# Kernel tuning notes

Measured on AMD Instinct MI355X. Metric: run time of the kernel, lower is better.

Reference implementation:

```python
import jax, jax.numpy as jnp
import numpy as np

B, T, D = 64, 128, 512  # batch, seq_len, d_model == memory_dim


def setup_inputs() -> dict:
    key = jax.random.key(0)
    ks = jax.random.split(key, 14)
    bound = 1.0 / np.sqrt(D)  # nn.Linear / kaiming_uniform(a=sqrt(5)) bound for fan_in=D
    u = lambda k, shape: jax.random.uniform(k, shape, jnp.float32, -bound, bound)
    return {
        "x": jax.random.normal(ks[0], (B, T, D), jnp.float32),
        "W_Q": u(ks[1], (D, D)),
        "W_K": u(ks[2], (D, D)),
        "W_V": u(ks[3], (D, D)),
        "theta_w": u(ks[4], (1, D)), "theta_b": u(ks[5], (1,)),
        "eta_w": u(ks[6], (1, D)), "eta_b": u(ks[7], (1,)),
        "alpha_w": u(ks[8], (1, D)), "alpha_b": u(ks[9], (1,)),
        "W1": u(ks[10], (D, D)), "b1": u(ks[11], (D,)),
        "W2": u(ks[12], (D, D)), "b2": u(ks[13], (D,)),
    }


def _run(x, W_Q, W_K, W_V, theta_w, theta_b, eta_w, eta_b, alpha_w, alpha_b,
         W1, b1, W2, b2):
    LO, HI = 1e-10, 1e10  # loss clamp range (grad passes through strictly inside)
    Bn, Tn, Dn = x.shape
    N = Bn * Dn  # mse_loss 'mean' normalizer over (batch, memory_dim)

    def step(carry, x_t):  # x_t: (B, D)
        cW1, cb1, cW2, cb2, M1w, M1b, M2w, M2b = carry
        # read path: q -> 2-layer memory MLP (relu, then linear)
        q = x_t @ W_Q.T
        mem = jax.nn.relu(q @ cW1.T + cb1) @ cW2.T + cb2
        # per-step scalar gates: mean over batch of sigmoid(proj(x_t))
        theta = jnp.mean(jax.nn.sigmoid(x_t @ theta_w.T + theta_b))
        eta = jnp.mean(jax.nn.sigmoid(x_t @ eta_w.T + eta_b))
        alpha = jnp.mean(jax.nn.sigmoid(x_t @ alpha_w.T + alpha_b))
        # write path: grad of clamped mean MSE( MLP(k), v ) wrt memory weights
        k = x_t @ W_K.T
        v = x_t @ W_V.T
        h_pre = k @ cW1.T + cb1
        h = jax.nn.relu(h_pre)
        out = h @ cW2.T + cb2
        diff = out - v
        loss = jnp.mean(diff * diff)
        pt = jnp.where((loss >= LO) & (loss <= HI), 1.0, 0.0)  # clamp passthrough
        dout = (pt * 2.0 / N) * diff                            # (B, D)
        gW2 = dout.T @ h
        gb2 = dout.sum(0)
        dpre = jnp.where(h_pre > 0, dout @ cW2, 0.0)
        gW1 = dpre.T @ k
        gb1 = dpre.sum(0)
        # momentum + weight decay update
        M1w = eta * M1w - theta * gW1
        M1b = eta * M1b - theta * gb1
        M2w = eta * M2w - theta * gW2
        M2b = eta * M2b - theta * gb2
        nW1 = (1.0 - alpha) * cW1 + M1w
        nb1 = (1.0 - alpha) * cb1 + M1b
        nW2 = (1.0 - alpha) * cW2 + M2w
        nb2 = (1.0 - alpha) * cb2 + M2b
        return (nW1, nb1, nW2, nb2, M1w, M1b, M2w, M2b), mem

    carry0 = (W1, b1, W2, b2,
              jnp.zeros_like(W1), jnp.zeros_like(b1),
              jnp.zeros_like(W2), jnp.zeros_like(b2))
    _, mem_seq = jax.lax.scan(step, carry0, jnp.swapaxes(x, 0, 1))  # (T, B, D)
    return jnp.swapaxes(mem_seq, 0, 1)  # (B, T, D)


def reference(x, W_Q, W_K, W_V, theta_w, theta_b, eta_w, eta_b, alpha_w, alpha_b,
              W1, b1, W2, b2):
    outputs = _run(x, W_Q, W_K, W_V, theta_w, theta_b, eta_w, eta_b,
                   alpha_w, alpha_b, W1, b1, W2, b2)
    # original returns (outputs, memory_outputs), which are identical tensors
    return (outputs, outputs)
```

## Files before the change

kernel.cpp:

```cpp
#include <hip/hip_runtime.h>
#include <stdint.h>


typedef __attribute__((ext_vector_type(8))) short short8;
typedef __attribute__((ext_vector_type(4))) float floatx4;

#define GBLK 16
#define SC_AGENT __HIP_MEMORY_SCOPE_AGENT

__device__ inline floatx4 mfma_bf16(short8 a, short8 b, floatx4 c) {
  return __builtin_amdgcn_mfma_f32_16x16x32_bf16(a, b, c, 0, 0, 0);
}
__device__ inline unsigned short f2bf(float f) {
  unsigned u = __float_as_uint(f);
  u += 0x7fffu + ((u >> 16) & 1u);
  return (unsigned short)(u >> 16);
}
__device__ inline float bf2f(unsigned short h) {
  return __uint_as_float(((unsigned)h) << 16);
}
__device__ inline short8 ldbf8(const unsigned short* p) {
  return *reinterpret_cast<const short8*>(p);
}
__device__ inline void stg16_sc(unsigned short* p, short8 v) {
  asm volatile("global_store_dwordx4 %0, %1, off sc0 sc1"
               :: "v"(p), "v"(v) : "memory");
}
__device__ inline void vmwait() {
  asm volatile("s_waitcnt vmcnt(0)" ::: "memory");
}
__device__ inline short8 ld16_sc(const unsigned short* p) {
  union { unsigned long long u[2]; short8 s; } c;
  c.u[0] = __hip_atomic_load(reinterpret_cast<const unsigned long long*>(p),
                             __ATOMIC_RELAXED, SC_AGENT);
  c.u[1] = __hip_atomic_load(reinterpret_cast<const unsigned long long*>(p + 4),
                             __ATOMIC_RELAXED, SC_AGENT);
  return c.s;
}
__device__ inline short8 pack8(const float* p) {
  float4 a = *reinterpret_cast<const float4*>(p);
  float4 b = *reinterpret_cast<const float4*>(p + 4);
  short8 r;
  r[0] = (short)f2bf(a.x); r[1] = (short)f2bf(a.y);
  r[2] = (short)f2bf(a.z); r[3] = (short)f2bf(a.w);
  r[4] = (short)f2bf(b.x); r[5] = (short)f2bf(b.y);
  r[6] = (short)f2bf(b.z); r[7] = (short)f2bf(b.w);
  return r;
}

__device__ inline void gridbar(unsigned* ctr, unsigned& ep) {
  vmwait();
  __syncthreads();
  if (threadIdx.x == 0) {
    __hip_atomic_fetch_add(ctr, 1u, __ATOMIC_RELAXED, SC_AGENT);
    const unsigned target = (ep + 1u) * GBLK;
    while (__hip_atomic_load(ctr, __ATOMIC_RELAXED, SC_AGENT) < target)
      __builtin_amdgcn_s_sleep(1);
  }
  ++ep;
  __syncthreads();
}

__global__ __launch_bounds__(256) void qkv_kernel(
    const float* __restrict__ x, const float* __restrict__ WQ,
    const float* __restrict__ WK, const float* __restrict__ WV,
    unsigned short* __restrict__ qb, unsigned short* __restrict__ kb,
    unsigned short* __restrict__ vb, unsigned short* __restrict__ kbT) {
  const int tid = threadIdx.x;
  const int lane = tid & 63, w = tid >> 6;
  const int quad = lane >> 4, l16 = lane & 15;
  const int Mbase = blockIdx.x * 128;
  const int Nbase = blockIdx.y * 128;
  const int z = blockIdx.z;
  const float* W = (z == 0) ? WQ : (z == 1) ? WK : WV;
  unsigned short* dst = (z == 0) ? qb : (z == 1) ? kb : vb;

  floatx4 acc[2][8];
  for (int a = 0; a < 2; ++a)
    for (int n = 0; n < 8; ++n) acc[a][n] = (floatx4){0.f, 0.f, 0.f, 0.f};

  const int r0 = Mbase + w * 32 + l16;
  for (int ks = 0; ks < 16; ++ks) {
    const int k0 = ks * 32 + quad * 8;
    short8 a0 = pack8(x + (size_t)r0 * 512 + k0);
    short8 a1 = pack8(x + (size_t)(r0 + 16) * 512 + k0);
    for (int n = 0; n < 8; ++n) {
      short8 b = pack8(W + (size_t)(Nbase + n * 16 + l16) * 512 + k0);
      acc[0][n] = mfma_bf16(a0, b, acc[0][n]);
      acc[1][n] = mfma_bf16(a1, b, acc[1][n]);
    }
  }
  for (int tm = 0; tm < 2; ++tm)
    for (int n = 0; n < 8; ++n)
      for (int rr = 0; rr < 4; ++rr) {
        int row = Mbase + w * 32 + tm * 16 + quad * 4 + rr;
        int col = Nbase + n * 16 + l16;
        int b = row >> 7, t = row & 127;
        unsigned short val = f2bf(acc[tm][n][rr]);
        dst[((size_t)(t * 64 + b) << 9) + col] = val;
        if (z == 1) kbT[((size_t)(t * 512 + col) << 6) + b] = val;
      }
}

__global__ __launch_bounds__(256) void gates_kernel(
    const float* __restrict__ x,
    const float* __restrict__ tw, const float* __restrict__ tb,
    const float* __restrict__ ew, const float* __restrict__ eb,
    const float* __restrict__ aw, const float* __restrict__ ab,
    float* __restrict__ gates, float* __restrict__ lossAcc,
    unsigned* __restrict__ ctr) {
  const int t = blockIdx.x, tid = threadIdx.x;
  __shared__ float red[192];
  if (tid < 192) {
    int g = tid >> 6, b = tid & 63;
    const float* wr = (g == 0) ? tw : (g == 1) ? ew : aw;
    float bias = (g == 0) ? tb[0] : (g == 1) ? eb[0] : ab[0];
    const float* xr = x + ((size_t)b * 128 + t) * 512;
    float s = 0.f;
    for (int i = 0; i < 512; i += 4) {
      float4 xv = *reinterpret_cast<const float4*>(xr + i);
      float4 wv = *reinterpret_cast<const float4*>(wr + i);
      s += xv.x * wv.x + xv.y * wv.y + xv.z * wv.z + xv.w * wv.w;
    }
    red[tid] = 1.f / (1.f + expf(-(s + bias)));
  }
  if (tid == 192) lossAcc[t] = 0.f;
  if (tid == 193 && t == 0) *ctr = 0u;
  __syncthreads();
  if (tid < 3) {
    float s = 0.f;
    for (int i = 0; i < 64; ++i) s += red[tid * 64 + i];
    gates[tid * 128 + t] = s * (1.f / 64.f);
  }
}

__global__ __launch_bounds__(512, 2) void scan_kernel(
    const unsigned short* __restrict__ qb, const unsigned short* __restrict__ kb,
    const unsigned short* __restrict__ vb, const unsigned short* __restrict__ kbT,
    const float* __restrict__ gates, float* lossAcc, unsigned* ctr,
    const float* __restrict__ inW1, const float* __restrict__ inb1,
    const float* __restrict__ inW2, const float* __restrict__ inb2,
    unsigned short* W2T, unsigned short* RcG, unsigned short* hT,
    unsigned short* dout_rm, float* __restrict__ out) {
  __shared__ unsigned short sW1[32 * 520];
  __shared__ unsigned short sW2[32 * 520];
  __shared__ unsigned short sWT[512 * 40];
  __shared__ unsigned short shl[32 * 72];
  __shared__ unsigned short sdt[32 * 72];
  __shared__ unsigned short sdp[32 * 72];
  __shared__ unsigned short sStA[128 * 32];
  __shared__ unsigned short sDR[64 * 32];
  __shared__ float sOutF[64 * 32];
  __shared__ float b1loc[32], b2loc[32], mb1[32], mb2[32];

  const int tid = threadIdx.x, bid = blockIdx.x;
  const int lane = tid & 63, w = tid >> 6;
  const int quad = lane >> 4, l16 = lane & 15;
  const int J = bid * 32;
  const int mt = w & 1, ng = w >> 1;
  const int mtc = w & 3, ntc = w >> 2;
  unsigned ep = 0;

  float w1s[32], m1s[32], w2s[32], m2s[32];
#pragma unroll
  for (int g = 0; g < 8; ++g) {
    unsigned short tp[4];
#pragma unroll
    for (int rr = 0; rr < 4; ++rr) {
      const int jl = mt * 16 + quad * 4 + rr;
      const int l = (ng * 8 + g) * 16 + l16;
      const int si = g * 4 + rr;
      const size_t gi = (size_t)(J + jl) * 512 + l;
      float a = inW1[gi]; w1s[si] = a; m1s[si] = 0.f; sW1[jl * 520 + l] = f2bf(a);
      float b = inW2[gi]; w2s[si] = b; m2s[si] = 0.f;
      unsigned short bb = f2bf(b);
      sW2[jl * 520 + l] = bb; tp[rr] = bb;
    }
    const int l = (ng * 8 + g) * 16 + l16;
    *reinterpret_cast<unsigned long long*>(&sWT[l * 40 + mt * 16 + quad * 4]) =
        (unsigned long long)tp[0] | ((unsigned long long)tp[1] << 16) |
        ((unsigned long long)tp[2] << 32) | ((unsigned long long)tp[3] << 48);
  }
  if (tid < 32) {
    b1loc[tid] = inb1[J + tid]; mb1[tid] = 0.f;
    b2loc[tid] = inb2[J + tid]; mb2[tid] = 0.f;
  }
  __syncthreads();
  {
#pragma unroll
    for (int ii = 0; ii < 4; ++ii) {
      const int r = w * 64 + ii * 16 + (lane >> 2), c = lane & 3;
      short8 v = *reinterpret_cast<const short8*>(&sWT[r * 40 + c * 8]);
      stg16_sc(W2T + (size_t)r * 512 + J + c * 8, v);
    }
  }

  for (int t = 0; t < 128; ++t) {
    const int par = t & 1, nxt = par ^ 1;
    const float th = gates[t], et = gates[128 + t], al = gates[256 + t];
    const float oma = 1.f - al;
    const unsigned short* qt = qb + ((size_t)t << 15);
    const unsigned short* kt = kb + ((size_t)t << 15);
    const unsigned short* vt = vb + ((size_t)t << 15);
    const unsigned short* ktT = kbT + ((size_t)t << 15);
    unsigned short* hTp = hT + par * 32768;
    const unsigned short* w2tp = W2T + (size_t)par * 262144;
    unsigned short* w2tn = W2T + (size_t)nxt * 262144;

    {
      const int row = w * 16 + l16;
      const unsigned short* arow = (row < 64) ? (qt + (size_t)row * 512)
                                              : (kt + (size_t)(row - 64) * 512);
      floatx4 a0 = {0.f,0.f,0.f,0.f}, a1 = {0.f,0.f,0.f,0.f};
#pragma unroll
      for (int half = 0; half < 2; ++half) {
        short8 af[8];
#pragma unroll
        for (int ks = 0; ks < 8; ++ks)
          af[ks] = ldbf8(arow + (half * 8 + ks) * 32 + quad * 8);
#pragma unroll
        for (int ks = 0; ks < 8; ++ks) {
          const int k0 = (half * 8 + ks) * 32 + quad * 8;
          short8 b0 = *reinterpret_cast<const short8*>(&sW1[l16 * 520 + k0]);
          short8 b1f = *reinterpret_cast<const short8*>(&sW1[(16 + l16) * 520 + k0]);
          a0 = mfma_bf16(af[ks], b0, a0);
          a1 = mfma_bf16(af[ks], b1f, a1);
        }
      }
      const float bi0 = b1loc[l16], bi1 = b1loc[16 + l16];
#pragma unroll
      for (int rr = 0; rr < 4; ++rr) {
        const int orow = w * 16 + quad * 4 + rr;
        float v0 = fmaxf(a0[rr] + bi0, 0.f);
        float v1 = fmaxf(a1[rr] + bi1, 0.f);
        unsigned short h0 = f2bf(v0), h1 = f2bf(v1);
        sStA[orow * 32 + l16] = h0;
        sStA[orow * 32 + 16 + l16] = h1;
        if (orow >= 64) {
          const int i = orow - 64;
          shl[l16 * 72 + i] = h0;
          shl[(16 + l16) * 72 + i] = h1;
        }
      }
      __syncthreads();
      {
        const int r = w * 16 + (lane >> 2), c = lane & 3;
        short8 v = *reinterpret_cast<const short8*>(&sStA[r * 32 + c * 8]);
        stg16_sc(RcG + (size_t)r * 512 + J + c * 8, v);
      }
      if (w < 4) {
        const int r = w * 8 + (lane >> 3), c = lane & 7;
        short8 v = *reinterpret_cast<const short8*>(&shl[r * 72 + c * 8]);
        stg16_sc(hTp + (size_t)(J + r) * 64 + c * 8, v);
      }
    }
    gridbar(ctr, ep);

    {
      const int row = w * 16 + l16;
      const unsigned short* arow = RcG + (size_t)row * 512;
      floatx4 a0 = {0.f,0.f,0.f,0.f}, a1 = {0.f,0.f,0.f,0.f};
#pragma unroll
      for (int half = 0; half < 2; ++half) {
        short8 af[8];
#pragma unroll
        for (int ks = 0; ks < 8; ++ks)
          af[ks] = ld16_sc(arow + (half * 8 + ks) * 32 + quad * 8);
#pragma unroll
        for (int ks = 0; ks < 8; ++ks) {
          const int k0 = (half * 8 + ks) * 32 + quad * 8;
          short8 b0 = *reinterpret_cast<const short8*>(&sW2[l16 * 520 + k0]);
          short8 b1f = *reinterpret_cast<const short8*>(&sW2[(16 + l16) * 520 + k0]);
          a0 = mfma_bf16(af[ks], b0, a0);
          a1 = mfma_bf16(af[ks], b1f, a1);
        }
      }
      const float bi0 = b2loc[l16], bi1 = b2loc[16 + l16];
      float lossp = 0.f;
#pragma unroll
      for (int rr = 0; rr < 4; ++rr) {
        const int orow = w * 16 + quad * 4 + rr;
        float o0 = a0[rr] + bi0, o1 = a1[rr] + bi1;
        if (orow < 64) {
          sOutF[orow * 32 + l16] = o0;
          sOutF[orow * 32 + 16 + l16] = o1;
        } else {
          const int i = orow - 64;
          float d0 = o0 - bf2f(vt[(size_t)i * 512 + J + l16]);
          float d1 = o1 - bf2f(vt[(size_t)i * 512 + J + 16 + l16]);
          lossp += d0 * d0 + d1 * d1;
          unsigned short q0 = f2bf(6.103515625e-5f * d0);
          unsigned short q1 = f2bf(6.103515625e-5f * d1);
          sDR[i * 32 + l16] = q0;
          sDR[i * 32 + 16 + l16] = q1;
          sdt[l16 * 72 + i] = q0;
          sdt[(16 + l16) * 72 + i] = q1;
        }
      }
      if (w < 4) {
#pragma unroll
        for (int ii = 0; ii < 2; ++ii) {
          const int r = w * 16 + ii * 8 + (lane >> 3), c = lane & 7;
          float4 v = *reinterpret_cast<const float4*>(&sOutF[r * 32 + c * 4]);
          float* o0p = out + ((size_t)r * 128 + t) * 512 + J + c * 4;
          *reinterpret_cast<float4*>(o0p) = v;
          *reinterpret_cast<float4*>(o0p + 4194304) = v;
        }
      } else {
        const int r = (w - 4) * 16 + (lane >> 2), c = lane & 3;
        short8 v = *reinterpret_cast<const short8*>(&sDR[r * 32 + c * 8]);
        stg16_sc(dout_rm + (size_t)r * 512 + J + c * 8, v);
      }
      if (w >= 4) {
        for (int off = 32; off > 0; off >>= 1) lossp += __shfl_down(lossp, off);
        if (lane == 0)
          __hip_atomic_fetch_add(lossAcc + t, lossp, __ATOMIC_RELAXED, SC_AGENT);
      }
    }
    gridbar(ctr, ep);

    const float loss =
        __hip_atomic_load(lossAcc + t, __ATOMIC_RELAXED, SC_AGENT) * (1.f / 32768.f);
    const float pt = (loss >= 1e-10f && loss <= 1e10f) ? 1.f : 0.f;

    {
      const unsigned short* arow = dout_rm + (size_t)(mtc * 16 + l16) * 512;
      const unsigned short* brow = w2tp + (size_t)(J + ntc * 16 + l16) * 512;
      floatx4 acc = {0.f,0.f,0.f,0.f};
#pragma unroll
      for (int half = 0; half < 2; ++half) {
        short8 afr[8], bfr[8];
#pragma unroll
        for (int ks = 0; ks < 8; ++ks) {
          const int k0 = (half * 8 + ks) * 32 + quad * 8;
          afr[ks] = ld16_sc(arow + k0);
          bfr[ks] = ld16_sc(brow + k0);
        }
#pragma unroll
        for (int ks = 0; ks < 8; ++ks) acc = mfma_bf16(afr[ks], bfr[ks], acc);
      }
#pragma unroll
      for (int rr = 0; rr < 4; ++rr) {
        const int i = mtc * 16 + quad * 4 + rr;
        const int jl = ntc * 16 + l16;
        unsigned short hb = shl[jl * 72 + i];
        sdp[jl * 72 + i] = (hb != 0) ? f2bf(acc[rr]) : (unsigned short)0;
      }
    }
    __syncthreads();

    {
      floatx4 acc1[8];
#pragma unroll
      for (int g = 0; g < 8; ++g) acc1[g] = (floatx4){0.f,0.f,0.f,0.f};
#pragma unroll
      for (int half = 0; half < 2; ++half) {
        short8 bfr[2][4];
#pragma unroll
        for (int ks = 0; ks < 2; ++ks)
#pragma unroll
          for (int g = 0; g < 4; ++g) {
            const int l = (ng * 8 + half * 4 + g) * 16 + l16;
            bfr[ks][g] = ldbf8(ktT + (size_t)l * 64 + ks * 32 + quad * 8);
          }
#pragma unroll
        for (int ks = 0; ks < 2; ++ks) {
          short8 af = *reinterpret_cast<const short8*>(
              &sdp[(mt * 16 + l16) * 72 + ks * 32 + quad * 8]);
#pragma unroll
          for (int g = 0; g < 4; ++g)
            acc1[half * 4 + g] = mfma_bf16(af, bfr[ks][g], acc1[half * 4 + g]);
        }
      }
#pragma unroll
      for (int g = 0; g < 8; ++g)
#pragma unroll
        for (int rr = 0; rr < 4; ++rr) {
          const int jl = mt * 16 + quad * 4 + rr;
          const int l = (ng * 8 + g) * 16 + l16;
          const int si = g * 4 + rr;
          float m = et * m1s[si] - th * (pt * acc1[g][rr]);
          float wv = oma * w1s[si] + m;
          m1s[si] = m; w1s[si] = wv;
          sW1[jl * 520 + l] = f2bf(wv);
        }
      if (tid < 32) {
        float s = 0.f;
        for (int i = 0; i < 64; ++i) s += bf2f(sdp[tid * 72 + i]);
        float m = et * mb1[tid] - th * (pt * s);
        float bv = oma * b1loc[tid] + m;
        mb1[tid] = m; b1loc[tid] = bv;
      }
    }

    {
      floatx4 acc2[8];
#pragma unroll
      for (int g = 0; g < 8; ++g) acc2[g] = (floatx4){0.f,0.f,0.f,0.f};
#pragma unroll
      for (int half = 0; half < 2; ++half) {
        short8 bfr[2][4];
#pragma unroll
        for (int ks = 0; ks < 2; ++ks)
#pragma unroll
          for (int g = 0; g < 4; ++g) {
            const int l = (ng * 8 + half * 4 + g) * 16 + l16;
            bfr[ks][g] = ld16_sc(hTp + (size_t)l * 64 + ks * 32 + quad * 8);
          }
#pragma unroll
        for (int ks = 0; ks < 2; ++ks) {
          short8 af = *reinterpret_cast<const short8*>(
              &sdt[(mt * 16 + l16) * 72 + ks * 32 + quad * 8]);
#pragma unroll
          for (int g = 0; g < 4; ++g)
            acc2[half * 4 + g] = mfma_bf16(af, bfr[ks][g], acc2[half * 4 + g]);
        }
      }
#pragma unroll
      for (int g = 0; g < 8; ++g) {
        unsigned short tp[4];
#pragma unroll
        for (int rr = 0; rr < 4; ++rr) {
          const int jl = mt * 16 + quad * 4 + rr;
          const int l = (ng * 8 + g) * 16 + l16;
          const int si = g * 4 + rr;
          float m = et * m2s[si] - th * (pt * acc2[g][rr]);
          float wv = oma * w2s[si] + m;
          m2s[si] = m; w2s[si] = wv;
          unsigned short bb = f2bf(wv);
          sW2[jl * 520 + l] = bb; tp[rr] = bb;
        }
        const int l = (ng * 8 + g) * 16 + l16;
        *reinterpret_cast<unsigned long long*>(&sWT[l * 40 + mt * 16 + quad * 4]) =
            (unsigned long long)tp[0] | ((unsigned long long)tp[1] << 16) |
            ((unsigned long long)tp[2] << 32) | ((unsigned long long)tp[3] << 48);
      }
      if (tid < 32) {
        float s = 0.f;
        for (int i = 0; i < 64; ++i) s += bf2f(sdt[tid * 72 + i]);
        float m = et * mb2[tid] - th * (pt * s);
        float bv = oma * b2loc[tid] + m;
        mb2[tid] = m; b2loc[tid] = bv;
      }
    }
    __syncthreads();

    {
#pragma unroll
      for (int ii = 0; ii < 4; ++ii) {
        const int r = w * 64 + ii * 16 + (lane >> 2), c = lane & 3;
        short8 v = *reinterpret_cast<const short8*>(&sWT[r * 40 + c * 8]);
        stg16_sc(w2tn + (size_t)r * 512 + J + c * 8, v);
      }
    }
    __syncthreads();
  }
  vmwait();
}

extern "C" void kernel_launch(void* const* d_in, const int* in_sizes, int n_in,
                              void* d_out, int out_size, void* d_ws, size_t ws_size,
                              hipStream_t stream) {
  const float* x  = (const float*)d_in[0];
  const float* WQ = (const float*)d_in[1];
  const float* WK = (const float*)d_in[2];
  const float* WV = (const float*)d_in[3];
  const float* tw = (const float*)d_in[4];
  const float* tb = (const float*)d_in[5];
  const float* ew = (const float*)d_in[6];
  const float* eb = (const float*)d_in[7];
  const float* aw = (const float*)d_in[8];
  const float* ab = (const float*)d_in[9];
  const float* W1 = (const float*)d_in[10];
  const float* b1 = (const float*)d_in[11];
  const float* W2 = (const float*)d_in[12];
  const float* b2 = (const float*)d_in[13];
  float* out = (float*)d_out;

  char* ws = (char*)d_ws;
  size_t off = 0;
  auto alloc = [&](size_t b) {
    char* p = ws + off;
    off = (off + b + 255) & ~(size_t)255;
    return p;
  };
  unsigned short* qb   = (unsigned short*)alloc(8388608);
  unsigned short* kb   = (unsigned short*)alloc(8388608);
  unsigned short* vb   = (unsigned short*)alloc(8388608);
  unsigned short* kbT  = (unsigned short*)alloc(8388608);
  float* gates   = (float*)alloc(1536);
  float* lossAcc = (float*)alloc(512);
  unsigned* ctr  = (unsigned*)alloc(256);
  unsigned short* W2T  = (unsigned short*)alloc(1048576);
  unsigned short* RcG  = (unsigned short*)alloc(131072);
  unsigned short* hT   = (unsigned short*)alloc(131072);
  unsigned short* dout_rm = (unsigned short*)alloc(65536);
  (void)in_sizes; (void)n_in; (void)out_size; (void)ws_size;

  qkv_kernel<<<dim3(64, 4, 3), 256, 0, stream>>>(x, WQ, WK, WV, qb, kb, vb, kbT);
  gates_kernel<<<dim3(128), 256, 0, stream>>>(x, tw, tb, ew, eb, aw, ab,
                                              gates, lossAcc, ctr);
  scan_kernel<<<dim3(GBLK), 512, 0, stream>>>(
      qb, kb, vb, kbT, gates, lossAcc, ctr,
      W1, b1, W2, b2,
      W2T, RcG, hT, dout_rm, out);
}
```

Measured before the change: 6.699 ms.

## Replace grid barriers with per-block flags and double-buffer scan exchange buffers

Swaps the counter-based grid barrier for per-block epoch flags that each wave polls with a wave vote. RcG and dout_rm are double-buffered by step parity so producers can run ahead without a full barrier. The output stores now sit between the signal and the wait, and v, k-transpose and h fragment loads are hoisted earlier so memory latency overlaps the synchronisation. A trailing __syncthreads is dropped. This relies on parity buffering and the flag ordering being enough to prevent cross-step races, and it uses more registers for the larger fragment arrays.

```diff
diff --git a/kernel.cpp b/kernel.cpp
--- a/kernel.cpp
+++ b/kernel.cpp
@@ -48,17 +48,21 @@
   return r;
 }
 
-__device__ inline void gridbar(unsigned* ctr, unsigned& ep) {
+__device__ inline void signal(unsigned* flag, unsigned val) {
   vmwait();
   __syncthreads();
-  if (threadIdx.x == 0) {
-    __hip_atomic_fetch_add(ctr, 1u, __ATOMIC_RELAXED, SC_AGENT);
-    const unsigned target = (ep + 1u) * GBLK;
-    while (__hip_atomic_load(ctr, __ATOMIC_RELAXED, SC_AGENT) < target)
-      __builtin_amdgcn_s_sleep(1);
-  }
-  ++ep;
-  __syncthreads();
+  if (threadIdx.x == 0)
+    __hip_atomic_store(flag, val, __ATOMIC_RELAXED, SC_AGENT);
+}
+__device__ inline void waitflags(const unsigned* f, unsigned target) {
+  const int lane = threadIdx.x & 63;
+  for (;;) {
+    unsigned v = target;
+    if (lane < GBLK)
+      v = __hip_atomic_load(f + lane, __ATOMIC_RELAXED, SC_AGENT);
+    if (__all(v >= target)) break;
+    __builtin_amdgcn_s_sleep(0);
+  }
 }
 
 __global__ __launch_bounds__(256) void qkv_kernel(
@@ -108,7 +112,7 @@
     const float* __restrict__ ew, const float* __restrict__ eb,
     const float* __restrict__ aw, const float* __restrict__ ab,
     float* __restrict__ gates, float* __restrict__ lossAcc,
-    unsigned* __restrict__ ctr) {
+    unsigned* __restrict__ flags) {
   const int t = blockIdx.x, tid = threadIdx.x;
   __shared__ float red[192];
   if (tid < 192) {
@@ -125,7 +129,7 @@
     red[tid] = 1.f / (1.f + expf(-(s + bias)));
   }
   if (tid == 192) lossAcc[t] = 0.f;
-  if (tid == 193 && t == 0) *ctr = 0u;
+  if (t == 0 && tid >= 200 && tid < 232) flags[tid - 200] = 0u;
   __syncthreads();
   if (tid < 3) {
     float s = 0.f;
@@ -137,7 +141,7 @@
 __global__ __launch_bounds__(512, 2) void scan_kernel(
     const unsigned short* __restrict__ qb, const unsigned short* __restrict__ kb,
     const unsigned short* __restrict__ vb, const unsigned short* __restrict__ kbT,
-    const float* __restrict__ gates, float* lossAcc, unsigned* ctr,
+    const float* __restrict__ gates, float* lossAcc, unsigned* flags,
     const float* __restrict__ inW1, const float* __restrict__ inb1,
     const float* __restrict__ inW2, const float* __restrict__ inb2,
     unsigned short* W2T, unsigned short* RcG, unsigned short* hT,
@@ -159,7 +163,8 @@
   const int J = bid * 32;
   const int mt = w & 1, ng = w >> 1;
   const int mtc = w & 3, ntc = w >> 2;
-  unsigned ep = 0;
+  unsigned* flagsA = flags;
+  unsigned* flagsB = flags + GBLK;
 
   float w1s[32], m1s[32], w2s[32], m2s[32];
 #pragma unroll
@@ -203,29 +208,37 @@
     const unsigned short* kt = kb + ((size_t)t << 15);
     const unsigned short* vt = vb + ((size_t)t << 15);
     const unsigned short* ktT = kbT + ((size_t)t << 15);
+    unsigned short* RcP = RcG + par * 65536;
+    unsigned short* doutP = dout_rm + par * 32768;
     unsigned short* hTp = hT + par * 32768;
     const unsigned short* w2tp = W2T + (size_t)par * 262144;
     unsigned short* w2tn = W2T + (size_t)nxt * 262144;
 
+    unsigned short vtr[8];
     {
       const int row = w * 16 + l16;
       const unsigned short* arow = (row < 64) ? (qt + (size_t)row * 512)
                                               : (kt + (size_t)(row - 64) * 512);
+      if (w >= 4) {
+#pragma unroll
+        for (int rr = 0; rr < 4; ++rr) {
+          const int i = (w - 4) * 16 + quad * 4 + rr;
+          vtr[rr] = vt[(size_t)i * 512 + J + l16];
+          vtr[4 + rr] = vt[(size_t)i * 512 + J + 16 + l16];
+        }
+      }
+      short8 af[16];
+#pragma unroll
+      for (int ks = 0; ks < 16; ++ks)
+        af[ks] = ldbf8(arow + ks * 32 + quad * 8);
       floatx4 a0 = {0.f,0.f,0.f,0.f}, a1 = {0.f,0.f,0.f,0.f};
 #pragma unroll
-      for (int half = 0; half < 2; ++half) {
-        short8 af[8];
-#pragma unroll
-        for (int ks = 0; ks < 8; ++ks)
-          af[ks] = ldbf8(arow + (half * 8 + ks) * 32 + quad * 8);
-#pragma unroll
-        for (int ks = 0; ks < 8; ++ks) {
-          const int k0 = (half * 8 + ks) * 32 + quad * 8;
-          short8 b0 = *reinterpret_cast<const short8*>(&sW1[l16 * 520 + k0]);
-          short8 b1f = *reinterpret_cast<const short8*>(&sW1[(16 + l16) * 520 + k0]);
-          a0 = mfma_bf16(af[ks], b0, a0);
-          a1 = mfma_bf16(af[ks], b1f, a1);
-        }
+      for (int ks = 0; ks < 16; ++ks) {
+        const int k0 = ks * 32 + quad * 8;
+        short8 b0 = *reinterpret_cast<const short8*>(&sW1[l16 * 520 + k0]);
+        short8 b1f = *reinterpret_cast<const short8*>(&sW1[(16 + l16) * 520 + k0]);
+        a0 = mfma_bf16(af[ks], b0, a0);
+        a1 = mfma_bf16(af[ks], b1f, a1);
       }
       const float bi0 = b1loc[l16], bi1 = b1loc[16 + l16];
 #pragma unroll
@@ -246,7 +259,7 @@
       {
         const int r = w * 16 + (lane >> 2), c = lane & 3;
         short8 v = *reinterpret_cast<const short8*>(&sStA[r * 32 + c * 8]);
-        stg16_sc(RcG + (size_t)r * 512 + J + c * 8, v);
+        stg16_sc(RcP + (size_t)r * 512 + J + c * 8, v);
       }
       if (w < 4) {
         const int r = w * 8 + (lane >> 3), c = lane & 7;
@@ -254,26 +267,24 @@
         stg16_sc(hTp + (size_t)(J + r) * 64 + c * 8, v);
       }
     }
-    gridbar(ctr, ep);
+    signal(flagsA + bid, t + 1);
 
     {
+      waitflags(flagsA, t + 1);
       const int row = w * 16 + l16;
-      const unsigned short* arow = RcG + (size_t)row * 512;
+      const unsigned short* arow = RcP + (size_t)row * 512;
+      short8 af[16];
+#pragma unroll
+      for (int ks = 0; ks < 16; ++ks)
+        af[ks] = ld16_sc(arow + ks * 32 + quad * 8);
       floatx4 a0 = {0.f,0.f,0.f,0.f}, a1 = {0.f,0.f,0.f,0.f};
 #pragma unroll
-      for (int half = 0; half < 2; ++half) {
-        short8 af[8];
-#pragma unroll
-        for (int ks = 0; ks < 8; ++ks)
-          af[ks] = ld16_sc(arow + (half * 8 + ks) * 32 + quad * 8);
-#pragma unroll
-        for (int ks = 0; ks < 8; ++ks) {
-          const int k0 = (half * 8 + ks) * 32 + quad * 8;
-          short8 b0 = *reinterpret_cast<const short8*>(&sW2[l16 * 520 + k0]);
-          short8 b1f = *reinterpret_cast<const short8*>(&sW2[(16 + l16) * 520 + k0]);
-          a0 = mfma_bf16(af[ks], b0, a0);
-          a1 = mfma_bf16(af[ks], b1f, a1);
-        }
+      for (int ks = 0; ks < 16; ++ks) {
+        const int k0 = ks * 32 + quad * 8;
+        short8 b0 = *reinterpret_cast<const short8*>(&sW2[l16 * 520 + k0]);
+        short8 b1f = *reinterpret_cast<const short8*>(&sW2[(16 + l16) * 520 + k0]);
+        a0 = mfma_bf16(af[ks], b0, a0);
+        a1 = mfma_bf16(af[ks], b1f, a1);
       }
       const float bi0 = b2loc[l16], bi1 = b2loc[16 + l16];
       float lossp = 0.f;
@@ -286,8 +297,8 @@
           sOutF[orow * 32 + 16 + l16] = o1;
         } else {
           const int i = orow - 64;
-          float d0 = o0 - bf2f(vt[(size_t)i * 512 + J + l16]);
-          float d1 = o1 - bf2f(vt[(size_t)i * 512 + J + 16 + l16]);
+          float d0 = o0 - bf2f(vtr[rr]);
+          float d1 = o1 - bf2f(vtr[4 + rr]);
           lossp += d0 * d0 + d1 * d1;
           unsigned short q0 = f2bf(6.103515625e-5f * d0);
           unsigned short q1 = f2bf(6.103515625e-5f * d1);
@@ -297,48 +308,45 @@
           sdt[(16 + l16) * 72 + i] = q1;
         }
       }
-      if (w < 4) {
-#pragma unroll
-        for (int ii = 0; ii < 2; ++ii) {
-          const int r = w * 16 + ii * 8 + (lane >> 3), c = lane & 7;
-          float4 v = *reinterpret_cast<const float4*>(&sOutF[r * 32 + c * 4]);
-          float* o0p = out + ((size_t)r * 128 + t) * 512 + J + c * 4;
-          *reinterpret_cast<float4*>(o0p) = v;
-          *reinterpret_cast<float4*>(o0p + 4194304) = v;
-        }
-      } else {
+      if (w >= 4) {
         const int r = (w - 4) * 16 + (lane >> 2), c = lane & 3;
         short8 v = *reinterpret_cast<const short8*>(&sDR[r * 32 + c * 8]);
-        stg16_sc(dout_rm + (size_t)r * 512 + J + c * 8, v);
-      }
-      if (w >= 4) {
+        stg16_sc(doutP + (size_t)r * 512 + J + c * 8, v);
         for (int off = 32; off > 0; off >>= 1) lossp += __shfl_down(lossp, off);
         if (lane == 0)
           __hip_atomic_fetch_add(lossAcc + t, lossp, __ATOMIC_RELAXED, SC_AGENT);
       }
     }
-    gridbar(ctr, ep);
-
-    const float loss =
-        __hip_atomic_load(lossAcc + t, __ATOMIC_RELAXED, SC_AGENT) * (1.f / 32768.f);
-    const float pt = (loss >= 1e-10f && loss <= 1e10f) ? 1.f : 0.f;
+    signal(flagsB + bid, t + 1);
+    if (w < 4) {
+#pragma unroll
+      for (int ii = 0; ii < 2; ++ii) {
+        const int r = w * 16 + ii * 8 + (lane >> 3), c = lane & 7;
+        float4 v = *reinterpret_cast<const float4*>(&sOutF[r * 32 + c * 4]);
+        float* o0p = out + ((size_t)r * 128 + t) * 512 + J + c * 4;
+        *reinterpret_cast<float4*>(o0p) = v;
+        *reinterpret_cast<float4*>(o0p + 4194304) = v;
+      }
+    }
 
     {
-      const unsigned short* arow = dout_rm + (size_t)(mtc * 16 + l16) * 512;
+      waitflags(flagsB, t + 1);
+      const unsigned short* arow = doutP + (size_t)(mtc * 16 + l16) * 512;
       const unsigned short* brow = w2tp + (size_t)(J + ntc * 16 + l16) * 512;
+      short8 afr[16], bfr[16];
+#pragma unroll
+      for (int ks = 0; ks < 16; ++ks) {
+        const int k0 = ks * 32 + quad * 8;
+        afr[ks] = ld16_sc(arow + k0);
+        bfr[ks] = ld16_sc(brow + k0);
+      }
+      const float loss =
+          __hip_atomic_load(lossAcc + t, __ATOMIC_RELAXED, SC_AGENT) *
+          (1.f / 32768.f);
+      const float pt = (loss >= 1e-10f && loss <= 1e10f) ? 1.f : 0.f;
       floatx4 acc = {0.f,0.f,0.f,0.f};
 #pragma unroll
-      for (int half = 0; half < 2; ++half) {
-        short8 afr[8], bfr[8];
-#pragma unroll
-        for (int ks = 0; ks < 8; ++ks) {
-          const int k0 = (half * 8 + ks) * 32 + quad * 8;
-          afr[ks] = ld16_sc(arow + k0);
-          bfr[ks] = ld16_sc(brow + k0);
-        }
-#pragma unroll
-        for (int ks = 0; ks < 8; ++ks) acc = mfma_bf16(afr[ks], bfr[ks], acc);
-      }
+      for (int ks = 0; ks < 16; ++ks) acc = mfma_bf16(afr[ks], bfr[ks], acc);
 #pragma unroll
       for (int rr = 0; rr < 4; ++rr) {
         const int i = mtc * 16 + quad * 4 + rr;
@@ -346,32 +354,31 @@
         unsigned short hb = shl[jl * 72 + i];
         sdp[jl * 72 + i] = (hb != 0) ? f2bf(acc[rr]) : (unsigned short)0;
       }
-    }
-    __syncthreads();
-
-    {
+      __syncthreads();
+
+      short8 kfr[16], hfr[16];
+#pragma unroll
+      for (int u = 0; u < 16; ++u) {
+        const int half = u >> 3, ks = (u >> 2) & 1, g = u & 3;
+        const int l = (ng * 8 + half * 4 + g) * 16 + l16;
+        kfr[u] = ldbf8(ktT + (size_t)l * 64 + ks * 32 + quad * 8);
+        hfr[u] = ld16_sc(hTp + (size_t)l * 64 + ks * 32 + quad * 8);
+      }
+
       floatx4 acc1[8];
 #pragma unroll
       for (int g = 0; g < 8; ++g) acc1[g] = (floatx4){0.f,0.f,0.f,0.f};
 #pragma unroll
-      for (int half = 0; half < 2; ++half) {
-        short8 bfr[2][4];
-#pragma unroll
-        for (int ks = 0; ks < 2; ++ks)
-#pragma unroll
-          for (int g = 0; g < 4; ++g) {
-            const int l = (ng * 8 + half * 4 + g) * 16 + l16;
-            bfr[ks][g] = ldbf8(ktT + (size_t)l * 64 + ks * 32 + quad * 8);
-          }
+      for (int half = 0; half < 2; ++half)
 #pragma unroll
         for (int ks = 0; ks < 2; ++ks) {
           short8 af = *reinterpret_cast<const short8*>(
               &sdp[(mt * 16 + l16) * 72 + ks * 32 + quad * 8]);
 #pragma unroll
           for (int g = 0; g < 4; ++g)
-            acc1[half * 4 + g] = mfma_bf16(af, bfr[ks][g], acc1[half * 4 + g]);
-        }
-      }
+            acc1[half * 4 + g] =
+                mfma_bf16(af, kfr[half * 8 + ks * 4 + g], acc1[half * 4 + g]);
+        }
 #pragma unroll
       for (int g = 0; g < 8; ++g)
 #pragma unroll
@@ -391,31 +398,21 @@
         float bv = oma * b1loc[tid] + m;
         mb1[tid] = m; b1loc[tid] = bv;
       }
-    }
-
-    {
+
       floatx4 acc2[8];
 #pragma unroll
       for (int g = 0; g < 8; ++g) acc2[g] = (floatx4){0.f,0.f,0.f,0.f};
 #pragma unroll
-      for (int half = 0; half < 2; ++half) {
-        short8 bfr[2][4];
-#pragma unroll
-        for (int ks = 0; ks < 2; ++ks)
-#pragma unroll
-          for (int g = 0; g < 4; ++g) {
-            const int l = (ng * 8 + half * 4 + g) * 16 + l16;
-            bfr[ks][g] = ld16_sc(hTp + (size_t)l * 64 + ks * 32 + quad * 8);
-          }
+      for (int half = 0; half < 2; ++half)
 #pragma unroll
         for (int ks = 0; ks < 2; ++ks) {
           short8 af = *reinterpret_cast<const short8*>(
               &sdt[(mt * 16 + l16) * 72 + ks * 32 + quad * 8]);
 #pragma unroll
           for (int g = 0; g < 4; ++g)
-            acc2[half * 4 + g] = mfma_bf16(af, bfr[ks][g], acc2[half * 4 + g]);
-        }
-      }
+            acc2[half * 4 + g] =
+                mfma_bf16(af, hfr[half * 8 + ks * 4 + g], acc2[half * 4 + g]);
+        }
 #pragma unroll
       for (int g = 0; g < 8; ++g) {
         unsigned short tp[4];
@@ -453,7 +450,6 @@
         stg16_sc(w2tn + (size_t)r * 512 + J + c * 8, v);
       }
     }
-    __syncthreads();
   }
   vmwait();
 }
@@ -490,18 +486,18 @@
   unsigned short* kbT  = (unsigned short*)alloc(8388608);
   float* gates   = (float*)alloc(1536);
   float* lossAcc = (float*)alloc(512);
-  unsigned* ctr  = (unsigned*)alloc(256);
+  unsigned* flags = (unsigned*)alloc(256);
   unsigned short* W2T  = (unsigned short*)alloc(1048576);
-  unsigned short* RcG  = (unsigned short*)alloc(131072);
+  unsigned short* RcG  = (unsigned short*)alloc(262144);
   unsigned short* hT   = (unsigned short*)alloc(131072);
-  unsigned short* dout_rm = (unsigned short*)alloc(65536);
+  unsigned short* dout_rm = (unsigned short*)alloc(131072);
   (void)in_sizes; (void)n_in; (void)out_size; (void)ws_size;
 
   qkv_kernel<<<dim3(64, 4, 3), 256, 0, stream>>>(x, WQ, WK, WV, qb, kb, vb, kbT);
   gates_kernel<<<dim3(128), 256, 0, stream>>>(x, tw, tb, ew, eb, aw, ab,
-                                              gates, lossAcc, ctr);
+                                              gates, lossAcc, flags);
   scan_kernel<<<dim3(GBLK), 512, 0, stream>>>(
-      qb, kb, vb, kbT, gates, lossAcc, ctr,
+      qb, kb, vb, kbT, gates, lossAcc, flags,
       W1, b1, W2, b2,
       W2T, RcG, hT, dout_rm, out);
 }
```

New measurement: 7.146 ms. 6.7% more time.
